# Kernel tuning notes

Hardware: AMD Instinct MI355X
Metric: run time of the kernel (lower is better)

Reference implementation:

```python
import jax, jax.numpy as jnp
import numpy as np
from jax import lax

NEG = -1e30  # finite stand-in for -inf (avoids NaN grads)
EPS = 1e-7   # keras backend epsilon used by ctc_batch_cost: log(y_pred + eps)

B, T, C, L = 64, 2048, 128, 256


def setup_inputs() -> dict:
    key = jax.random.key(0)
    k1, k2 = jax.random.split(key)
    # labels in [0, C-2]; blank index is C-1 per keras ctc_batch_cost convention
    y_true = jax.random.randint(k1, (B, L), 0, C - 1, dtype=jnp.int32).astype(jnp.int64)
    # y_pred are (unnormalized) per-frame class probabilities, as keras expects softmax output
    y_pred = jax.random.uniform(k2, (B, T, C), dtype=jnp.float32)
    return {"y_true": y_true, "y_pred": y_pred}


def _lse3(a, b, c):
    s = jnp.stack([a, b, c], axis=0)
    m = jnp.max(s, axis=0)
    return m + jnp.log(jnp.sum(jnp.exp(s - m), axis=0))


def _ctc_loss(y_true, y_pred):
    """Faithful jnp version of K.ctc_batch_cost with full input/label lengths."""
    b, t, c = y_pred.shape
    l = y_true.shape[1]
    blank = c - 1
    S = 2 * l + 1

    logp = jnp.log(y_pred + EPS)  # [B,T,C]

    labels = y_true.astype(jnp.int32)
    # extended label sequence: blank, l1, blank, l2, ..., blank  -> [B,S]
    ext = jnp.full((b, S), blank, dtype=jnp.int32).at[:, 1::2].set(labels)
    # gather per-frame log-probs of extended labels -> [B,T,S]
    lp_z = jnp.take_along_axis(logp, jnp.broadcast_to(ext[:, None, :], (b, t, S)), axis=2)

    # skip transition allowed at s if z[s] != blank and z[s] != z[s-2]
    ext_m2 = jnp.concatenate([jnp.full((b, 2), blank, jnp.int32), ext[:, :-2]], axis=1)
    skip = (ext != blank) & (ext != ext_m2) & (jnp.arange(S)[None, :] >= 2)  # [B,S]

    lp_tbs = jnp.transpose(lp_z, (1, 0, 2))  # [T,B,S]

    neg = jnp.full((b, S), NEG, dtype=logp.dtype)
    alpha0 = neg.at[:, 0].set(lp_tbs[0][:, 0]).at[:, 1].set(lp_tbs[0][:, 1])

    neg1 = jnp.full((b, 1), NEG, dtype=logp.dtype)
    neg2 = jnp.full((b, 2), NEG, dtype=logp.dtype)

    def step(alpha, lp_t):
        s1 = jnp.concatenate([neg1, alpha[:, :-1]], axis=1)
        s2 = jnp.where(skip, jnp.concatenate([neg2, alpha[:, :-2]], axis=1), NEG)
        new = _lse3(alpha, s1, s2) + lp_t
        return new, None

    alphaT, _ = lax.scan(step, alpha0, lp_tbs[1:])
    loss = -jnp.logaddexp(alphaT[:, -1], alphaT[:, -2])  # [B]
    return loss[:, None]  # keras ctc_batch_cost returns [B,1]


def reference(y_true, y_pred):
    return _ctc_loss(y_true, y_pred)
```

## Files before the change

### kernel.cpp

```cpp
#include <hip/hip_runtime.h>


#define B_ 64
#define T_ 2048
#define C_ 128
#define L_ 256
#define BLANK_ (C_ - 1)
#define EPSF 1e-7f
#define LN2F 0.69314718055994530942f
#define CH_ 16
#define SENT_ (-(1 << 28))

typedef __attribute__((address_space(1))) const void glob_cv;
typedef __attribute__((address_space(3))) void lds_v;
typedef __attribute__((address_space(3))) float lds_f;

__device__ __forceinline__ void gl2lds16(const void* g, void* l) {
    __builtin_amdgcn_global_load_lds((glob_cv*)g, (lds_v*)l, 16, 0, 0);
}

#define WAIT_VM(n) asm volatile("s_waitcnt vmcnt(" #n ")" ::: "memory")
#define DRAIN_LGKM() asm volatile("s_waitcnt lgkmcnt(0)" ::: "memory")

#define XS_(x) #x
#define XS(x) XS_(x)

#define FILLC(S, OFF) \
  "ds_read_b32 %[g" #S "b], %[cB] offset:" XS(OFF) "\n\t" \
  "ds_read_b32 %[g" #S "1], %[c1] offset:" XS(OFF) "\n\t" \
  "ds_read_b32 %[g" #S "3], %[c3] offset:" XS(OFF) "\n\t" \
  "ds_read_b32 %[g" #S "5], %[c5] offset:" XS(OFF) "\n\t" \
  "ds_read_b32 %[g" #S "7], %[c7] offset:" XS(OFF) "\n\t"
#define FILLN(S, OFF) \
  "ds_read_b32 %[g" #S "b], %[nB] offset:" XS(OFF) "\n\t" \
  "ds_read_b32 %[g" #S "1], %[n1] offset:" XS(OFF) "\n\t" \
  "ds_read_b32 %[g" #S "3], %[n3] offset:" XS(OFF) "\n\t" \
  "ds_read_b32 %[g" #S "5], %[n5] offset:" XS(OFF) "\n\t" \
  "ds_read_b32 %[g" #S "7], %[n7] offset:" XS(OFF) "\n\t"

#define STEPF(S, WN, FILLS) \
  "s_waitcnt lgkmcnt(" XS(WN) ")\n\t" \
  "v_mov_b32 %[t0], 0\n\t" \
  "v_add_f32 %[t1], 0x33d6bf95, %[g" #S "b]\n\t" \
  "v_add_f32 %[t2], 0x33d6bf95, %[g" #S "1]\n\t" \
  "v_add_f32 %[t3], 0x33d6bf95, %[g" #S "3]\n\t" \
  "v_add_f32 %[t4], 0x33d6bf95, %[g" #S "5]\n\t" \
  "v_add_f32 %[t5], 0x33d6bf95, %[g" #S "7]\n\t" \
  "v_mov_b32_dpp %[t0], %[va7] wave_shr:1 row_mask:0xf bank_mask:0xf\n\t" \
  "v_mul_f32 %[t0], %[t0], %[ups]\n\t" \
  "v_add_f32 %[t6], %[va0], %[va1]\n\t" \
  "v_fmac_f32 %[t6], %[m1], %[t0]\n\t" \
  "v_add_f32 %[va0], %[va0], %[t0]\n\t" \
  "v_mul_f32 %[va0], %[va0], %[t1]\n\t" \
  "v_add_f32 %[t7], %[va1], %[va2]\n\t" \
  "v_add_f32 %[t8], %[va2], %[va3]\n\t" \
  "v_fmac_f32 %[t8], %[m3], %[va1]\n\t" \
  "v_mul_f32 %[va1], %[t6], %[t2]\n\t" \
  "v_mul_f32 %[va2], %[t7], %[t1]\n\t" \
  "v_add_f32 %[t6], %[va3], %[va4]\n\t" \
  "v_add_f32 %[t7], %[va4], %[va5]\n\t" \
  "v_fmac_f32 %[t7], %[m5], %[va3]\n\t" \
  "v_mul_f32 %[va3], %[t8], %[t3]\n\t" \
  "v_mul_f32 %[va4], %[t6], %[t1]\n\t" \
  "v_add_f32 %[t6], %[va5], %[va6]\n\t" \
  "v_add_f32 %[t8], %[va6], %[va7]\n\t" \
  "v_fmac_f32 %[t8], %[m7], %[va5]\n\t" \
  "v_mul_f32 %[va5], %[t7], %[t4]\n\t" \
  "v_mul_f32 %[va6], %[t6], %[t1]\n\t" \
  "v_fmac_f32 %[va8], %[m8], %[va7]\n\t" \
  "v_mul_f32 %[va7], %[t8], %[t5]\n\t" \
  "v_mul_f32 %[va8], %[va8], %[t1]\n\t" \
  FILLS

#define STEPB(S, WN, FILLS) \
  "s_waitcnt lgkmcnt(" XS(WN) ")\n\t" \
  "v_mov_b32 %[t0], 0\n\t" \
  "v_add_f32 %[t1], 0x33d6bf95, %[g" #S "b]\n\t" \
  "v_add_f32 %[t2], 0x33d6bf95, %[g" #S "1]\n\t" \
  "v_add_f32 %[t3], 0x33d6bf95, %[g" #S "3]\n\t" \
  "v_add_f32 %[t4], 0x33d6bf95, %[g" #S "5]\n\t" \
  "v_add_f32 %[t5], 0x33d6bf95, %[g" #S "7]\n\t" \
  "v_mul_f32 %[va0], %[va0], %[t1]\n\t" \
  "v_mul_f32 %[va1], %[va1], %[t2]\n\t" \
  "v_mov_b32 %[t6], %[va0]\n\t" \
  "v_fmac_f32 %[t6], %[m1], %[va1]\n\t" \
  "v_mul_f32 %[va2], %[va2], %[t1]\n\t" \
  "v_mul_f32 %[va3], %[va3], %[t3]\n\t" \
  "v_mul_f32 %[va4], %[va4], %[t1]\n\t" \
  "v_mov_b32_dpp %[t0], %[t6] wave_shl:1 row_mask:0xf bank_mask:0xf\n\t" \
  "v_mul_f32 %[t0], %[t0], %[ups]\n\t" \
  "v_mul_f32 %[va5], %[va5], %[t4]\n\t" \
  "v_mul_f32 %[va6], %[va6], %[t1]\n\t" \
  "v_mul_f32 %[va7], %[va7], %[t5]\n\t" \
  "v_mul_f32 %[va8], %[va8], %[t1]\n\t" \
  "v_add_f32 %[t7], %[va1], %[va2]\n\t" \
  "v_fmac_f32 %[t7], %[m3], %[va3]\n\t" \
  "v_add_f32 %[va0], %[va0], %[va1]\n\t" \
  "v_add_f32 %[t8], %[va3], %[va4]\n\t" \
  "v_fmac_f32 %[t8], %[m5], %[va5]\n\t" \
  "v_add_f32 %[va2], %[va2], %[va3]\n\t" \
  "v_add_f32 %[t9], %[va5], %[va6]\n\t" \
  "v_fmac_f32 %[t9], %[m7], %[va7]\n\t" \
  "v_add_f32 %[va4], %[va4], %[va5]\n\t" \
  "v_add_f32 %[va6], %[va6], %[va7]\n\t" \
  "v_add_f32 %[va7], %[va7], %[t0]\n\t" \
  "v_fmac_f32 %[va7], %[m8], %[va8]\n\t" \
  "v_mov_b32 %[va1], %[t7]\n\t" \
  "v_mov_b32 %[va3], %[t8]\n\t" \
  "v_mov_b32 %[va5], %[t9]\n\t" \
  FILLS

#define BDY_HEAD \
  "v_max_f32 %[t1], %[va0], %[va1]\n\t" \
  "v_max_f32 %[t2], %[va2], %[va3]\n\t" \
  "v_max_f32 %[t3], %[va4], %[va5]\n\t" \
  "v_max_f32 %[t4], %[va6], %[va7]\n\t" \
  "v_max_f32 %[t1], %[t1], %[t2]\n\t" \
  "v_max_f32 %[t3], %[t3], %[t4]\n\t" \
  "v_max_f32 %[t1], %[t1], %[t3]\n\t" \
  "v_max_f32 %[t1], %[t1], %[va8]\n\t" \
  "v_cmp_ne_u32 vcc, 0, %[t1]\n\t" \
  "v_lshrrev_b32 %[t2], 23, %[t1]\n\t" \
  "v_sub_u32 %[t3], 0xfe, %[t2]\n\t" \
  "v_lshlrev_b32 %[t3], 23, %[t3]\n\t" \
  "v_cndmask_b32 %[t3], 1.0, %[t3], vcc\n\t" \
  "v_mul_f32 %[va0], %[va0], %[t3]\n\t" \
  "v_mul_f32 %[va1], %[va1], %[t3]\n\t" \
  "v_mul_f32 %[va2], %[va2], %[t3]\n\t" \
  "v_mul_f32 %[va3], %[va3], %[t3]\n\t" \
  "v_mul_f32 %[va4], %[va4], %[t3]\n\t" \
  "v_mul_f32 %[va5], %[va5], %[t3]\n\t" \
  "v_mul_f32 %[va6], %[va6], %[t3]\n\t" \
  "v_mul_f32 %[va7], %[va7], %[t3]\n\t" \
  "v_mul_f32 %[va8], %[va8], %[t3]\n\t" \
  "v_add_u32 %[t2], 0xffffff81, %[t2]\n\t" \
  "v_add_u32 %[t2], %[E], %[t2]\n\t" \
  "v_mov_b32 %[t4], 0xf0000000\n\t" \
  "v_cndmask_b32 %[E], %[t4], %[t2], vcc\n\t" \
  "v_mov_b32 %[t5], 0xf0000000\n\t" \
  "s_nop 1\n\t"
#define BDY_TAIL \
  "v_cmp_ne_u32 vcc, 0xf0000000, %[E]\n\t" \
  "v_cndmask_b32 %[E], %[t5], %[E], vcc\n\t" \
  "v_sub_u32 %[t6], %[t5], %[E]\n\t" \
  "v_max_i32 %[t6], 0xffffff82, %[t6]\n\t" \
  "v_min_i32 %[t6], 0x78, %[t6]\n\t" \
  "v_add_u32 %[t6], 0x7f, %[t6]\n\t" \
  "v_lshlrev_b32 %[ups], 23, %[t6]\n\t"
#define BDYF BDY_HEAD \
  "v_mov_b32_dpp %[t5], %[E] wave_shr:1 row_mask:0xf bank_mask:0xf\n\t" \
  BDY_TAIL
#define BDYB BDY_HEAD \
  "v_mov_b32_dpp %[t5], %[E] wave_shl:1 row_mask:0xf bank_mask:0xf\n\t" \
  BDY_TAIL

#define FWD_Q1 STEPF(0,15,FILLC(0,2048)) STEPF(1,15,FILLC(1,2560)) \
               STEPF(2,15,FILLC(2,3072)) STEPF(3,15,FILLC(3,3584)) BDYF
#define FWD_Q2 STEPF(0,15,FILLC(0,4096)) STEPF(1,15,FILLC(1,4608)) \
               STEPF(2,15,FILLC(2,5120)) STEPF(3,15,FILLC(3,5632)) BDYF
#define FWD_Q3 STEPF(0,15,FILLC(0,6144)) STEPF(1,15,FILLC(1,6656)) \
               STEPF(2,15,FILLC(2,7168)) STEPF(3,15,FILLC(3,7680)) BDYF
#define FWD_Q4 STEPF(0,15,FILLN(0,0))    STEPF(1,15,FILLN(1,512)) \
               STEPF(2,15,FILLN(2,1024)) STEPF(3,15,FILLN(3,1536)) BDYF
#define FWD_FULL_BODY FWD_Q1 FWD_Q2 FWD_Q3 FWD_Q4
#define FWD_FIRST_BODY \
  FILLC(1,512) FILLC(2,1024) FILLC(3,1536) FILLC(0,2048) \
  STEPF(1,15,FILLC(1,2560)) STEPF(2,15,FILLC(2,3072)) \
  STEPF(3,15,FILLC(3,3584)) BDYF \
  FWD_Q2 FWD_Q3 FWD_Q4
#define FWD_LAST_BODY FWD_Q1 FWD_Q2 FWD_Q3 \
  STEPF(0,15,"") STEPF(1,10,"") STEPF(2,5,"") STEPF(3,0,"") BDYF

#define BWD_Q1 STEPB(0,15,FILLC(0,5632)) STEPB(1,15,FILLC(1,5120)) \
               STEPB(2,15,FILLC(2,4608)) STEPB(3,15,FILLC(3,4096)) BDYB
#define BWD_Q2 STEPB(0,15,FILLC(0,3584)) STEPB(1,15,FILLC(1,3072)) \
               STEPB(2,15,FILLC(2,2560)) STEPB(3,15,FILLC(3,2048)) BDYB
#define BWD_Q3 STEPB(0,15,FILLC(0,1536)) STEPB(1,15,FILLC(1,1024)) \
               STEPB(2,15,FILLC(2,512))  STEPB(3,15,FILLC(3,0))    BDYB
#define BWD_Q4 STEPB(0,15,FILLN(0,7680)) STEPB(1,15,FILLN(1,7168)) \
               STEPB(2,15,FILLN(2,6656)) STEPB(3,15,FILLN(3,6144)) BDYB
#define BWD_FULL_BODY BWD_Q1 BWD_Q2 BWD_Q3 BWD_Q4
#define BWD_FIRST_BODY \
  FILLC(0,7680) FILLC(1,7168) FILLC(2,6656) FILLC(3,6144) \
  BWD_FULL_BODY
#define BWD_LAST_BODY BWD_Q1 BWD_Q2 BWD_Q3 \
  STEPB(0,15,"") STEPB(1,10,"") STEPB(2,5,"") STEPB(3,0,"") BDYB

#define ST_OUTS \
  [va0]"+&v"(a0),[va1]"+&v"(a1),[va2]"+&v"(a2),[va3]"+&v"(a3), \
  [va4]"+&v"(a4),[va5]"+&v"(a5),[va6]"+&v"(a6),[va7]"+&v"(a7), \
  [va8]"+&v"(a8),[E]"+&v"(E),[ups]"+&v"(ups), \
  [g0b]"+&v"(g0b),[g01]"+&v"(g01),[g03]"+&v"(g03),[g05]"+&v"(g05),[g07]"+&v"(g07), \
  [g1b]"+&v"(g1b),[g11]"+&v"(g11),[g13]"+&v"(g13),[g15]"+&v"(g15),[g17]"+&v"(g17), \
  [g2b]"+&v"(g2b),[g21]"+&v"(g21),[g23]"+&v"(g23),[g25]"+&v"(g25),[g27]"+&v"(g27), \
  [g3b]"+&v"(g3b),[g31]"+&v"(g31),[g33]"+&v"(g33),[g35]"+&v"(g35),[g37]"+&v"(g37), \
  [t0]"=&v"(t0),[t1]"=&v"(t1),[t2]"=&v"(t2),[t3]"=&v"(t3),[t4]"=&v"(t4), \
  [t5]"=&v"(t5),[t6]"=&v"(t6),[t7]"=&v"(t7),[t8]"=&v"(t8),[t9]"=&v"(t9)

#define RUN_CHUNK(BODY, XB,X1,X3,X5,X7, YB,Y1,Y3,Y5,Y7) \
  asm volatile(BODY : ST_OUTS \
    : [m1]"v"(m1f),[m3]"v"(m3f),[m5]"v"(m5f),[m7]"v"(m7f),[m8]"v"(m8f), \
      [cB]"v"(XB),[c1]"v"(X1),[c3]"v"(X3),[c5]"v"(X5),[c7]"v"(X7), \
      [nB]"v"(YB),[n1]"v"(Y1),[n3]"v"(Y3),[n5]"v"(Y5),[n7]"v"(Y7) \
    : "vcc","memory")

#define RUN_BDY(BODY) asm volatile(BODY : ST_OUTS :: "vcc","memory")

__launch_bounds__(128, 1)
__global__ void ctc_loss_kernel(const int* __restrict__ y_true,
                                const float* __restrict__ y_pred,
                                float* __restrict__ out) {
    const int b = blockIdx.x;
    const int tid = threadIdx.x;
    const int w = __builtin_amdgcn_readfirstlane(tid >> 6);
    const int l = tid & 63;

    __shared__ float ring[2][4][CH_ * C_];

    const int* __restrict__ lab = y_true + b * L_;
    const int4 lv = *(const int4*)(lab + 4 * l);
    const int e1 = lv.x, e3 = lv.y, e5 = lv.z, e7 = lv.w;
    const int em1 = (l > 0) ? lab[4 * l - 1] : -1;
    const float m1f = ((l > 0) && (e1 != em1)) ? 1.0f : 0.0f;
    const float m3f = (e3 != e1) ? 1.0f : 0.0f;
    const float m5f = (e5 != e3) ? 1.0f : 0.0f;
    const float m7f = (e7 != e5) ? 1.0f : 0.0f;
    const float m8f = (l == 63) ? 1.0f : 0.0f;

    const float* __restrict__ base = y_pred + (size_t)b * (T_ * C_);

    lds_f* lb = (lds_f*)&ring[0][0][0];
    lds_f* q0 = lb + w * 8192;
    lds_f* q1 = q0 + 2048;
    lds_f* q2 = q0 + 4096;
    lds_f* q3 = q0 + 6144;
    lds_f *cB0 = q0 + BLANK_, *c10 = q0 + e1, *c30 = q0 + e3,
          *c50 = q0 + e5, *c70 = q0 + e7;
    lds_f *cB1 = q1 + BLANK_, *c11 = q1 + e1, *c31 = q1 + e3,
          *c51 = q1 + e5, *c71 = q1 + e7;
    lds_f *cB2 = q2 + BLANK_, *c12 = q2 + e1, *c32 = q2 + e3,
          *c52 = q2 + e5, *c72 = q2 + e7;
    lds_f *cB3 = q3 + BLANK_, *c13 = q3 + e1, *c33 = q3 + e3,
          *c53 = q3 + e5, *c73 = q3 + e7;

    auto issueF = [&](int c, int buf) {
        const float* g = base + (size_t)c * CH_ * C_ + 4 * l;
#pragma unroll
        for (int i = 0; i < 8; ++i)
            gl2lds16(g + i * 256, &ring[0][buf][i * 256]);
    };
    auto issueB = [&](int qc, int buf) {
        const float* g = base + (size_t)(127 - qc) * CH_ * C_ + 4 * l;
#pragma unroll
        for (int i = 0; i < 8; ++i)
            gl2lds16(g + i * 256, &ring[1][buf][i * 256]);
    };

    float a0 = 0.f, a1 = 0.f, a2 = 0.f, a3 = 0.f, a4 = 0.f,
          a5 = 0.f, a6 = 0.f, a7 = 0.f, a8 = 0.f;
    int E = SENT_;
    float ups = 1.0f;
    float g0b = 0.f, g01 = 0.f, g03 = 0.f, g05 = 0.f, g07 = 0.f,
          g1b = 0.f, g11 = 0.f, g13 = 0.f, g15 = 0.f, g17 = 0.f,
          g2b = 0.f, g21 = 0.f, g23 = 0.f, g25 = 0.f, g27 = 0.f,
          g3b = 0.f, g31 = 0.f, g33 = 0.f, g35 = 0.f, g37 = 0.f;
    float t0, t1, t2, t3, t4, t5, t6, t7, t8, t9;

    if (w == 0) {
        issueF(0, 0); issueF(1, 1); issueF(2, 2);
        WAIT_VM(8);
        issueF(3, 3);
        {
            const float* rbf = &ring[0][0][0];
            const float i0 = rbf[BLANK_] + EPSF;
            const float i1 = rbf[e1] + EPSF;
            if (l == 0) { a0 = i0; a1 = i1; E = 0; }
        }
        RUN_BDY(BDYF);
        DRAIN_LGKM();
        RUN_CHUNK(FWD_FIRST_BODY, cB0,c10,c30,c50,c70, cB1,c11,c31,c51,c71);
        WAIT_VM(8); issueF(4, 0);
        RUN_CHUNK(FWD_FULL_BODY, cB1,c11,c31,c51,c71, cB2,c12,c32,c52,c72);
        WAIT_VM(8); issueF(5, 1);
        RUN_CHUNK(FWD_FULL_BODY, cB2,c12,c32,c52,c72, cB3,c13,c33,c53,c73);
        WAIT_VM(8); issueF(6, 2);
        RUN_CHUNK(FWD_FULL_BODY, cB3,c13,c33,c53,c73, cB0,c10,c30,c50,c70);
#pragma unroll 1
        for (int m = 1; m <= 14; ++m) {
            WAIT_VM(8); issueF(4 * m + 3, 3);
            RUN_CHUNK(FWD_FULL_BODY, cB0,c10,c30,c50,c70, cB1,c11,c31,c51,c71);
            WAIT_VM(8); issueF(4 * m + 4, 0);
            RUN_CHUNK(FWD_FULL_BODY, cB1,c11,c31,c51,c71, cB2,c12,c32,c52,c72);
            WAIT_VM(8); issueF(4 * m + 5, 1);
            RUN_CHUNK(FWD_FULL_BODY, cB2,c12,c32,c52,c72, cB3,c13,c33,c53,c73);
            WAIT_VM(8); issueF(4 * m + 6, 2);
            RUN_CHUNK(FWD_FULL_BODY, cB3,c13,c33,c53,c73, cB0,c10,c30,c50,c70);
        }
        WAIT_VM(8); issueF(63, 3);
        RUN_CHUNK(FWD_FULL_BODY, cB0,c10,c30,c50,c70, cB1,c11,c31,c51,c71);
        WAIT_VM(8);
        RUN_CHUNK(FWD_FULL_BODY, cB1,c11,c31,c51,c71, cB2,c12,c32,c52,c72);
        WAIT_VM(0);
        RUN_CHUNK(FWD_FULL_BODY, cB2,c12,c32,c52,c72, cB3,c13,c33,c53,c73);
        RUN_CHUNK(FWD_LAST_BODY, cB3,c13,c33,c53,c73, cB3,c13,c33,c53,c73);
    } else {
        issueB(0, 0); issueB(1, 1); issueB(2, 2);
        WAIT_VM(8);
        issueB(3, 3);
        if (l == 63) { a7 = 1.0f; a8 = 1.0f; E = 0; }
        RUN_BDY(BDYB);
        DRAIN_LGKM();
        RUN_CHUNK(BWD_FIRST_BODY, cB0,c10,c30,c50,c70, cB1,c11,c31,c51,c71);
        WAIT_VM(8); issueB(4, 0);
        RUN_CHUNK(BWD_FULL_BODY, cB1,c11,c31,c51,c71, cB2,c12,c32,c52,c72);
        WAIT_VM(8); issueB(5, 1);
        RUN_CHUNK(BWD_FULL_BODY, cB2,c12,c32,c52,c72, cB3,c13,c33,c53,c73);
        WAIT_VM(8); issueB(6, 2);
        RUN_CHUNK(BWD_FULL_BODY, cB3,c13,c33,c53,c73, cB0,c10,c30,c50,c70);
#pragma unroll 1
        for (int m = 1; m <= 14; ++m) {
            WAIT_VM(8); issueB(4 * m + 3, 3);
            RUN_CHUNK(BWD_FULL_BODY, cB0,c10,c30,c50,c70, cB1,c11,c31,c51,c71);
            WAIT_VM(8); issueB(4 * m + 4, 0);
            RUN_CHUNK(BWD_FULL_BODY, cB1,c11,c31,c51,c71, cB2,c12,c32,c52,c72);
            WAIT_VM(8); issueB(4 * m + 5, 1);
            RUN_CHUNK(BWD_FULL_BODY, cB2,c12,c32,c52,c72, cB3,c13,c33,c53,c73);
            WAIT_VM(8); issueB(4 * m + 6, 2);
            RUN_CHUNK(BWD_FULL_BODY, cB3,c13,c33,c53,c73, cB0,c10,c30,c50,c70);
        }
        WAIT_VM(8); issueB(63, 3);
        RUN_CHUNK(BWD_FULL_BODY, cB0,c10,c30,c50,c70, cB1,c11,c31,c51,c71);
        WAIT_VM(8);
        RUN_CHUNK(BWD_FULL_BODY, cB1,c11,c31,c51,c71, cB2,c12,c32,c52,c72);
        WAIT_VM(0);
        RUN_CHUNK(BWD_FULL_BODY, cB2,c12,c32,c52,c72, cB3,c13,c33,c53,c73);
        RUN_CHUNK(BWD_LAST_BODY, cB3,c13,c33,c53,c73, cB3,c13,c33,c53,c73);
        float* xf = &ring[1][0][0];
        xf[0 * 64 + l] = a0; xf[1 * 64 + l] = a1; xf[2 * 64 + l] = a2;
        xf[3 * 64 + l] = a3; xf[4 * 64 + l] = a4; xf[5 * 64 + l] = a5;
        xf[6 * 64 + l] = a6; xf[7 * 64 + l] = a7; xf[8 * 64 + l] = a8;
        ((int*)xf)[9 * 64 + l] = E;
    }

    __syncthreads();

    if (w == 0) {
        const float* xf = &ring[1][0][0];
        float sd = a0 * xf[0 * 64 + l];
        sd = fmaf(a1, xf[1 * 64 + l], sd);
        sd = fmaf(a2, xf[2 * 64 + l], sd);
        sd = fmaf(a3, xf[3 * 64 + l], sd);
        sd = fmaf(a4, xf[4 * 64 + l], sd);
        sd = fmaf(a5, xf[5 * 64 + l], sd);
        sd = fmaf(a6, xf[6 * 64 + l], sd);
        sd = fmaf(a7, xf[7 * 64 + l], sd);
        sd = fmaf(a8, xf[8 * 64 + l], sd);
        const int E2 = ((const int*)xf)[9 * 64 + l];
        const bool nz = (sd > 0.0f);
        int Es = nz ? (E + E2) : SENT_;
        int M = Es;
#pragma unroll
        for (int o = 32; o; o >>= 1) M = max(M, __shfl_xor(M, o));
        int d = Es - M;
        d = max(d, -126);
        float val = nz ? sd * __uint_as_float((unsigned)(d + 127) << 23) : 0.0f;
#pragma unroll
        for (int o = 32; o; o >>= 1) val += __shfl_xor(val, o);
        if (l == 0) out[b] = -(__logf(val) + (float)M * LN2F);
    }
}

extern "C" void kernel_launch(void* const* d_in, const int* in_sizes, int n_in,
                              void* d_out, int out_size, void* d_ws, size_t ws_size,
                              hipStream_t stream) {
    const int* y_true = (const int*)d_in[0];
    const float* y_pred = (const float*)d_in[1];
    float* out = (float*)d_out;
    ctc_loss_kernel<<<B_, 128, 0, stream>>>(y_true, y_pred, out);
}
```

Measured before the change: 184.6 us.

## Fold renormalization scale into next step's emission multiply and use fast boundary in late chunks

Adds a cheaper boundary renormalization variant that skips the zero/sentinel checks and uses max3. It defers applying the scale by folding it into the next step's emission factors through an FMA (g*sc + eps*sc). The fast boundary is used only in the later half of the time loop, where every lane is assumed to have left the all-zero sentinel state. It also removes extra moves and temporaries in the backward step and waits on LDS every other step. The risk is correctness if any lane still holds zeros or a sentinel exponent when the fast path begins.

```diff
diff --git a/kernel.cpp b/kernel.cpp
--- a/kernel.cpp
+++ b/kernel.cpp
@@ -24,6 +24,9 @@
 
 #define XS_(x) #x
 #define XS(x) XS_(x)
+
+#define WLG(n) "s_waitcnt lgkmcnt(" #n ")\n\t"
+#define NW ""
 
 #define FILLC(S, OFF) \
   "ds_read_b32 %[g" #S "b], %[cB] offset:" XS(OFF) "\n\t" \
@@ -38,16 +41,9 @@
   "ds_read_b32 %[g" #S "5], %[n5] offset:" XS(OFF) "\n\t" \
   "ds_read_b32 %[g" #S "7], %[n7] offset:" XS(OFF) "\n\t"
 
-#define STEPF(S, WN, FILLS) \
-  "s_waitcnt lgkmcnt(" XS(WN) ")\n\t" \
-  "v_mov_b32 %[t0], 0\n\t" \
-  "v_add_f32 %[t1], 0x33d6bf95, %[g" #S "b]\n\t" \
-  "v_add_f32 %[t2], 0x33d6bf95, %[g" #S "1]\n\t" \
-  "v_add_f32 %[t3], 0x33d6bf95, %[g" #S "3]\n\t" \
-  "v_add_f32 %[t4], 0x33d6bf95, %[g" #S "5]\n\t" \
-  "v_add_f32 %[t5], 0x33d6bf95, %[g" #S "7]\n\t" \
-  "v_mov_b32_dpp %[t0], %[va7] wave_shr:1 row_mask:0xf bank_mask:0xf\n\t" \
-  "v_mul_f32 %[t0], %[t0], %[ups]\n\t" \
+#define FCORE \
+  "v_mov_b32_dpp %[z0], %[va7] wave_shr:1 row_mask:0xf bank_mask:0xf\n\t" \
+  "v_mul_f32 %[t0], %[z0], %[ups]\n\t" \
   "v_add_f32 %[t6], %[va0], %[va1]\n\t" \
   "v_fmac_f32 %[t6], %[m1], %[t0]\n\t" \
   "v_add_f32 %[va0], %[va0], %[t0]\n\t" \
@@ -69,45 +65,68 @@
   "v_mul_f32 %[va6], %[t6], %[t1]\n\t" \
   "v_fmac_f32 %[va8], %[m8], %[va7]\n\t" \
   "v_mul_f32 %[va7], %[t8], %[t5]\n\t" \
-  "v_mul_f32 %[va8], %[va8], %[t1]\n\t" \
-  FILLS
-
-#define STEPB(S, WN, FILLS) \
-  "s_waitcnt lgkmcnt(" XS(WN) ")\n\t" \
-  "v_mov_b32 %[t0], 0\n\t" \
+  "v_mul_f32 %[va8], %[va8], %[t1]\n\t"
+
+#define STEPF(S, W, FILLS) W \
   "v_add_f32 %[t1], 0x33d6bf95, %[g" #S "b]\n\t" \
   "v_add_f32 %[t2], 0x33d6bf95, %[g" #S "1]\n\t" \
   "v_add_f32 %[t3], 0x33d6bf95, %[g" #S "3]\n\t" \
   "v_add_f32 %[t4], 0x33d6bf95, %[g" #S "5]\n\t" \
   "v_add_f32 %[t5], 0x33d6bf95, %[g" #S "7]\n\t" \
+  FCORE FILLS
+
+#define STEPF1(S, W, FILLS) W \
+  "v_fma_f32 %[t1], %[g" #S "b], %[sc], %[esc]\n\t" \
+  "v_fma_f32 %[t2], %[g" #S "1], %[sc], %[esc]\n\t" \
+  "v_fma_f32 %[t3], %[g" #S "3], %[sc], %[esc]\n\t" \
+  "v_fma_f32 %[t4], %[g" #S "5], %[sc], %[esc]\n\t" \
+  "v_fma_f32 %[t5], %[g" #S "7], %[sc], %[esc]\n\t" \
+  FCORE \
+  "v_mov_b32 %[ups], %[upn]\n\t" \
+  FILLS
+
+#define BCORE(UPSREG) \
   "v_mul_f32 %[va0], %[va0], %[t1]\n\t" \
   "v_mul_f32 %[va1], %[va1], %[t2]\n\t" \
-  "v_mov_b32 %[t6], %[va0]\n\t" \
-  "v_fmac_f32 %[t6], %[m1], %[va1]\n\t" \
+  "v_fma_f32 %[t6], %[m1], %[va1], %[va0]\n\t" \
   "v_mul_f32 %[va2], %[va2], %[t1]\n\t" \
   "v_mul_f32 %[va3], %[va3], %[t3]\n\t" \
   "v_mul_f32 %[va4], %[va4], %[t1]\n\t" \
-  "v_mov_b32_dpp %[t0], %[t6] wave_shl:1 row_mask:0xf bank_mask:0xf\n\t" \
-  "v_mul_f32 %[t0], %[t0], %[ups]\n\t" \
   "v_mul_f32 %[va5], %[va5], %[t4]\n\t" \
   "v_mul_f32 %[va6], %[va6], %[t1]\n\t" \
   "v_mul_f32 %[va7], %[va7], %[t5]\n\t" \
   "v_mul_f32 %[va8], %[va8], %[t1]\n\t" \
-  "v_add_f32 %[t7], %[va1], %[va2]\n\t" \
-  "v_fmac_f32 %[t7], %[m3], %[va3]\n\t" \
+  "v_mov_b32_dpp %[z0], %[t6] wave_shl:1 row_mask:0xf bank_mask:0xf\n\t" \
+  "v_mul_f32 %[t0], %[z0], " UPSREG "\n\t" \
   "v_add_f32 %[va0], %[va0], %[va1]\n\t" \
-  "v_add_f32 %[t8], %[va3], %[va4]\n\t" \
-  "v_fmac_f32 %[t8], %[m5], %[va5]\n\t" \
+  "v_add_f32 %[va1], %[va1], %[va2]\n\t" \
+  "v_fmac_f32 %[va1], %[m3], %[va3]\n\t" \
   "v_add_f32 %[va2], %[va2], %[va3]\n\t" \
-  "v_add_f32 %[t9], %[va5], %[va6]\n\t" \
-  "v_fmac_f32 %[t9], %[m7], %[va7]\n\t" \
+  "v_add_f32 %[va3], %[va3], %[va4]\n\t" \
+  "v_fmac_f32 %[va3], %[m5], %[va5]\n\t" \
   "v_add_f32 %[va4], %[va4], %[va5]\n\t" \
+  "v_add_f32 %[va5], %[va5], %[va6]\n\t" \
+  "v_fmac_f32 %[va5], %[m7], %[va7]\n\t" \
   "v_add_f32 %[va6], %[va6], %[va7]\n\t" \
   "v_add_f32 %[va7], %[va7], %[t0]\n\t" \
-  "v_fmac_f32 %[va7], %[m8], %[va8]\n\t" \
-  "v_mov_b32 %[va1], %[t7]\n\t" \
-  "v_mov_b32 %[va3], %[t8]\n\t" \
-  "v_mov_b32 %[va5], %[t9]\n\t" \
+  "v_fmac_f32 %[va7], %[m8], %[va8]\n\t"
+
+#define STEPB(S, W, FILLS) W \
+  "v_add_f32 %[t1], 0x33d6bf95, %[g" #S "b]\n\t" \
+  "v_add_f32 %[t2], 0x33d6bf95, %[g" #S "1]\n\t" \
+  "v_add_f32 %[t3], 0x33d6bf95, %[g" #S "3]\n\t" \
+  "v_add_f32 %[t4], 0x33d6bf95, %[g" #S "5]\n\t" \
+  "v_add_f32 %[t5], 0x33d6bf95, %[g" #S "7]\n\t" \
+  BCORE("%[ups]") FILLS
+
+#define STEPB1(S, W, FILLS) W \
+  "v_fma_f32 %[t1], %[g" #S "b], %[sc], %[esc]\n\t" \
+  "v_fma_f32 %[t2], %[g" #S "1], %[sc], %[esc]\n\t" \
+  "v_fma_f32 %[t3], %[g" #S "3], %[sc], %[esc]\n\t" \
+  "v_fma_f32 %[t4], %[g" #S "5], %[sc], %[esc]\n\t" \
+  "v_fma_f32 %[t5], %[g" #S "7], %[sc], %[esc]\n\t" \
+  BCORE("%[upn]") \
+  "v_mov_b32 %[ups], %[upn]\n\t" \
   FILLS
 
 #define BDY_HEAD \
@@ -146,56 +165,90 @@
   "v_max_i32 %[t6], 0xffffff82, %[t6]\n\t" \
   "v_min_i32 %[t6], 0x78, %[t6]\n\t" \
   "v_add_u32 %[t6], 0x7f, %[t6]\n\t" \
-  "v_lshlrev_b32 %[ups], 23, %[t6]\n\t"
-#define BDYF BDY_HEAD \
+  "v_lshlrev_b32 %[ups], 23, %[t6]\n\t" \
+  "v_mov_b32 %[sc], 1.0\n\t" \
+  "v_mov_b32 %[esc], 0x33d6bf95\n\t" \
+  "v_mov_b32 %[upn], %[ups]\n\t"
+#define BDYF_FULL BDY_HEAD \
   "v_mov_b32_dpp %[t5], %[E] wave_shr:1 row_mask:0xf bank_mask:0xf\n\t" \
   BDY_TAIL
-#define BDYB BDY_HEAD \
+#define BDYB_FULL BDY_HEAD \
   "v_mov_b32_dpp %[t5], %[E] wave_shl:1 row_mask:0xf bank_mask:0xf\n\t" \
   BDY_TAIL
 
-#define FWD_Q1 STEPF(0,15,FILLC(0,2048)) STEPF(1,15,FILLC(1,2560)) \
-               STEPF(2,15,FILLC(2,3072)) STEPF(3,15,FILLC(3,3584)) BDYF
-#define FWD_Q2 STEPF(0,15,FILLC(0,4096)) STEPF(1,15,FILLC(1,4608)) \
-               STEPF(2,15,FILLC(2,5120)) STEPF(3,15,FILLC(3,5632)) BDYF
-#define FWD_Q3 STEPF(0,15,FILLC(0,6144)) STEPF(1,15,FILLC(1,6656)) \
-               STEPF(2,15,FILLC(2,7168)) STEPF(3,15,FILLC(3,7680)) BDYF
-#define FWD_Q4 STEPF(0,15,FILLN(0,0))    STEPF(1,15,FILLN(1,512)) \
-               STEPF(2,15,FILLN(2,1024)) STEPF(3,15,FILLN(3,1536)) BDYF
-#define FWD_FULL_BODY FWD_Q1 FWD_Q2 FWD_Q3 FWD_Q4
+#define FBDY_HEAD \
+  "v_max3_f32 %[t1], %[va0], %[va1], %[va2]\n\t" \
+  "v_max3_f32 %[t2], %[va3], %[va4], %[va5]\n\t" \
+  "v_max3_f32 %[t3], %[va6], %[va7], %[va8]\n\t" \
+  "v_max3_f32 %[t1], %[t1], %[t2], %[t3]\n\t" \
+  "v_lshrrev_b32 %[t2], 23, %[t1]\n\t" \
+  "v_add_u32 %[t4], 0xffffff81, %[t2]\n\t" \
+  "v_add_u32 %[E], %[E], %[t4]\n\t" \
+  "v_sub_u32 %[t3], 0xfe, %[t2]\n\t" \
+  "v_lshlrev_b32 %[sc], 23, %[t3]\n\t" \
+  "v_mul_f32 %[esc], 0x33d6bf95, %[sc]\n\t"
+#define FBDY_TAIL \
+  "v_sub_u32 %[t4], %[t5], %[E]\n\t" \
+  "v_max_i32 %[t4], 0xffffff82, %[t4]\n\t" \
+  "v_min_i32 %[t4], 0x78, %[t4]\n\t" \
+  "v_add_u32 %[t4], 0x7f, %[t4]\n\t" \
+  "v_lshlrev_b32 %[upn], 23, %[t4]\n\t"
+#define BDYF_FAST FBDY_HEAD \
+  "v_mov_b32_dpp %[t5], %[E] wave_shr:1 row_mask:0xf bank_mask:0xf\n\t" \
+  FBDY_TAIL
+#define BDYB_FAST FBDY_HEAD \
+  "v_mov_b32_dpp %[t5], %[E] wave_shl:1 row_mask:0xf bank_mask:0xf\n\t" \
+  FBDY_TAIL
+
+#define FQ1(BDY) STEPF1(0,WLG(10),FILLC(0,2048)) STEPF(1,NW,FILLC(1,2560)) \
+                 STEPF(2,WLG(10),FILLC(2,3072)) STEPF(3,NW,FILLC(3,3584)) BDY
+#define FQ2(BDY) STEPF1(0,WLG(10),FILLC(0,4096)) STEPF(1,NW,FILLC(1,4608)) \
+                 STEPF(2,WLG(10),FILLC(2,5120)) STEPF(3,NW,FILLC(3,5632)) BDY
+#define FQ3(BDY) STEPF1(0,WLG(10),FILLC(0,6144)) STEPF(1,NW,FILLC(1,6656)) \
+                 STEPF(2,WLG(10),FILLC(2,7168)) STEPF(3,NW,FILLC(3,7680)) BDY
+#define FQ4(BDY) STEPF1(0,WLG(10),FILLN(0,0))    STEPF(1,NW,FILLN(1,512)) \
+                 STEPF(2,WLG(10),FILLN(2,1024)) STEPF(3,NW,FILLN(3,1536)) BDY
+
+#define FWD_FULL_BODY FQ1(BDYF_FULL) FQ2(BDYF_FULL) FQ3(BDYF_FULL) FQ4(BDYF_FULL)
+#define FWD_FAST_BODY FQ1(BDYF_FAST) FQ2(BDYF_FAST) FQ3(BDYF_FAST) FQ4(BDYF_FAST)
 #define FWD_FIRST_BODY \
   FILLC(1,512) FILLC(2,1024) FILLC(3,1536) FILLC(0,2048) \
-  STEPF(1,15,FILLC(1,2560)) STEPF(2,15,FILLC(2,3072)) \
-  STEPF(3,15,FILLC(3,3584)) BDYF \
-  FWD_Q2 FWD_Q3 FWD_Q4
-#define FWD_LAST_BODY FWD_Q1 FWD_Q2 FWD_Q3 \
-  STEPF(0,15,"") STEPF(1,10,"") STEPF(2,5,"") STEPF(3,0,"") BDYF
-
-#define BWD_Q1 STEPB(0,15,FILLC(0,5632)) STEPB(1,15,FILLC(1,5120)) \
-               STEPB(2,15,FILLC(2,4608)) STEPB(3,15,FILLC(3,4096)) BDYB
-#define BWD_Q2 STEPB(0,15,FILLC(0,3584)) STEPB(1,15,FILLC(1,3072)) \
-               STEPB(2,15,FILLC(2,2560)) STEPB(3,15,FILLC(3,2048)) BDYB
-#define BWD_Q3 STEPB(0,15,FILLC(0,1536)) STEPB(1,15,FILLC(1,1024)) \
-               STEPB(2,15,FILLC(2,512))  STEPB(3,15,FILLC(3,0))    BDYB
-#define BWD_Q4 STEPB(0,15,FILLN(0,7680)) STEPB(1,15,FILLN(1,7168)) \
-               STEPB(2,15,FILLN(2,6656)) STEPB(3,15,FILLN(3,6144)) BDYB
-#define BWD_FULL_BODY BWD_Q1 BWD_Q2 BWD_Q3 BWD_Q4
+  STEPF1(1,WLG(10),FILLC(1,2560)) STEPF(2,NW,FILLC(2,3072)) \
+  STEPF(3,WLG(10),FILLC(3,3584)) BDYF_FULL \
+  FQ2(BDYF_FULL) FQ3(BDYF_FULL) FQ4(BDYF_FULL)
+#define FWD_LAST_BODY FQ1(BDYF_FAST) FQ2(BDYF_FAST) FQ3(BDYF_FAST) \
+  STEPF1(0,WLG(10),"") STEPF(1,NW,"") STEPF(2,WLG(5),"") STEPF(3,WLG(0),"") \
+  BDYF_FULL
+
+#define BQ1(BDY) STEPB1(0,WLG(10),FILLC(0,5632)) STEPB(1,NW,FILLC(1,5120)) \
+                 STEPB(2,WLG(10),FILLC(2,4608)) STEPB(3,NW,FILLC(3,4096)) BDY
+#define BQ2(BDY) STEPB1(0,WLG(10),FILLC(0,3584)) STEPB(1,NW,FILLC(1,3072)) \
+                 STEPB(2,WLG(10),FILLC(2,2560)) STEPB(3,NW,FILLC(3,2048)) BDY
+#define BQ3(BDY) STEPB1(0,WLG(10),FILLC(0,1536)) STEPB(1,NW,FILLC(1,1024)) \
+                 STEPB(2,WLG(10),FILLC(2,512))  STEPB(3,NW,FILLC(3,0))    BDY
+#define BQ4(BDY) STEPB1(0,WLG(10),FILLN(0,7680)) STEPB(1,NW,FILLN(1,7168)) \
+                 STEPB(2,WLG(10),FILLN(2,6656)) STEPB(3,NW,FILLN(3,6144)) BDY
+
+#define BWD_FULL_BODY BQ1(BDYB_FULL) BQ2(BDYB_FULL) BQ3(BDYB_FULL) BQ4(BDYB_FULL)
+#define BWD_FAST_BODY BQ1(BDYB_FAST) BQ2(BDYB_FAST) BQ3(BDYB_FAST) BQ4(BDYB_FAST)
 #define BWD_FIRST_BODY \
   FILLC(0,7680) FILLC(1,7168) FILLC(2,6656) FILLC(3,6144) \
   BWD_FULL_BODY
-#define BWD_LAST_BODY BWD_Q1 BWD_Q2 BWD_Q3 \
-  STEPB(0,15,"") STEPB(1,10,"") STEPB(2,5,"") STEPB(3,0,"") BDYB
+#define BWD_LAST_BODY BQ1(BDYB_FAST) BQ2(BDYB_FAST) BQ3(BDYB_FAST) \
+  STEPB1(0,WLG(10),"") STEPB(1,NW,"") STEPB(2,WLG(5),"") STEPB(3,WLG(0),"") \
+  BDYB_FULL
 
 #define ST_OUTS \
   [va0]"+&v"(a0),[va1]"+&v"(a1),[va2]"+&v"(a2),[va3]"+&v"(a3), \
   [va4]"+&v"(a4),[va5]"+&v"(a5),[va6]"+&v"(a6),[va7]"+&v"(a7), \
-  [va8]"+&v"(a8),[E]"+&v"(E),[ups]"+&v"(ups), \
+  [va8]"+&v"(a8),[E]"+&v"(E),[ups]"+&v"(ups),[upn]"+&v"(upn), \
+  [sc]"+&v"(sc),[esc]"+&v"(esc),[z0]"+&v"(z0), \
   [g0b]"+&v"(g0b),[g01]"+&v"(g01),[g03]"+&v"(g03),[g05]"+&v"(g05),[g07]"+&v"(g07), \
   [g1b]"+&v"(g1b),[g11]"+&v"(g11),[g13]"+&v"(g13),[g15]"+&v"(g15),[g17]"+&v"(g17), \
   [g2b]"+&v"(g2b),[g21]"+&v"(g21),[g23]"+&v"(g23),[g25]"+&v"(g25),[g27]"+&v"(g27), \
   [g3b]"+&v"(g3b),[g31]"+&v"(g31),[g33]"+&v"(g33),[g35]"+&v"(g35),[g37]"+&v"(g37), \
   [t0]"=&v"(t0),[t1]"=&v"(t1),[t2]"=&v"(t2),[t3]"=&v"(t3),[t4]"=&v"(t4), \
-  [t5]"=&v"(t5),[t6]"=&v"(t6),[t7]"=&v"(t7),[t8]"=&v"(t8),[t9]"=&v"(t9)
+  [t5]"=&v"(t5),[t6]"=&v"(t6),[t7]"=&v"(t7),[t8]"=&v"(t8)
 
 #define RUN_CHUNK(BODY, XB,X1,X3,X5,X7, YB,Y1,Y3,Y5,Y7) \
   asm volatile(BODY : ST_OUTS \
@@ -259,12 +312,12 @@
     float a0 = 0.f, a1 = 0.f, a2 = 0.f, a3 = 0.f, a4 = 0.f,
           a5 = 0.f, a6 = 0.f, a7 = 0.f, a8 = 0.f;
     int E = SENT_;
-    float ups = 1.0f;
+    float ups = 1.0f, upn = 1.0f, sc = 1.0f, esc = EPSF, z0 = 0.0f;
     float g0b = 0.f, g01 = 0.f, g03 = 0.f, g05 = 0.f, g07 = 0.f,
           g1b = 0.f, g11 = 0.f, g13 = 0.f, g15 = 0.f, g17 = 0.f,
           g2b = 0.f, g21 = 0.f, g23 = 0.f, g25 = 0.f, g27 = 0.f,
           g3b = 0.f, g31 = 0.f, g33 = 0.f, g35 = 0.f, g37 = 0.f;
-    float t0, t1, t2, t3, t4, t5, t6, t7, t8, t9;
+    float t0, t1, t2, t3, t4, t5, t6, t7, t8;
 
     if (w == 0) {
         issueF(0, 0); issueF(1, 1); issueF(2, 2);
@@ -276,7 +329,7 @@
             const float i1 = rbf[e1] + EPSF;
             if (l == 0) { a0 = i0; a1 = i1; E = 0; }
         }
-        RUN_BDY(BDYF);
+        RUN_BDY(BDYF_FULL);
         DRAIN_LGKM();
         RUN_CHUNK(FWD_FIRST_BODY, cB0,c10,c30,c50,c70, cB1,c11,c31,c51,c71);
         WAIT_VM(8); issueF(4, 0);
@@ -286,7 +339,7 @@
         WAIT_VM(8); issueF(6, 2);
         RUN_CHUNK(FWD_FULL_BODY, cB3,c13,c33,c53,c73, cB0,c10,c30,c50,c70);
 #pragma unroll 1
-        for (int m = 1; m <= 14; ++m) {
+        for (int m = 1; m <= 6; ++m) {
             WAIT_VM(8); issueF(4 * m + 3, 3);
             RUN_CHUNK(FWD_FULL_BODY, cB0,c10,c30,c50,c70, cB1,c11,c31,c51,c71);
             WAIT_VM(8); issueF(4 * m + 4, 0);
@@ -296,19 +349,30 @@
             WAIT_VM(8); issueF(4 * m + 6, 2);
             RUN_CHUNK(FWD_FULL_BODY, cB3,c13,c33,c53,c73, cB0,c10,c30,c50,c70);
         }
+#pragma unroll 1
+        for (int m = 7; m <= 14; ++m) {
+            WAIT_VM(8); issueF(4 * m + 3, 3);
+            RUN_CHUNK(FWD_FAST_BODY, cB0,c10,c30,c50,c70, cB1,c11,c31,c51,c71);
+            WAIT_VM(8); issueF(4 * m + 4, 0);
+            RUN_CHUNK(FWD_FAST_BODY, cB1,c11,c31,c51,c71, cB2,c12,c32,c52,c72);
+            WAIT_VM(8); issueF(4 * m + 5, 1);
+            RUN_CHUNK(FWD_FAST_BODY, cB2,c12,c32,c52,c72, cB3,c13,c33,c53,c73);
+            WAIT_VM(8); issueF(4 * m + 6, 2);
+            RUN_CHUNK(FWD_FAST_BODY, cB3,c13,c33,c53,c73, cB0,c10,c30,c50,c70);
+        }
         WAIT_VM(8); issueF(63, 3);
-        RUN_CHUNK(FWD_FULL_BODY, cB0,c10,c30,c50,c70, cB1,c11,c31,c51,c71);
+        RUN_CHUNK(FWD_FAST_BODY, cB0,c10,c30,c50,c70, cB1,c11,c31,c51,c71);
         WAIT_VM(8);
-        RUN_CHUNK(FWD_FULL_BODY, cB1,c11,c31,c51,c71, cB2,c12,c32,c52,c72);
+        RUN_CHUNK(FWD_FAST_BODY, cB1,c11,c31,c51,c71, cB2,c12,c32,c52,c72);
         WAIT_VM(0);
-        RUN_CHUNK(FWD_FULL_BODY, cB2,c12,c32,c52,c72, cB3,c13,c33,c53,c73);
+        RUN_CHUNK(FWD_FAST_BODY, cB2,c12,c32,c52,c72, cB3,c13,c33,c53,c73);
         RUN_CHUNK(FWD_LAST_BODY, cB3,c13,c33,c53,c73, cB3,c13,c33,c53,c73);
     } else {
         issueB(0, 0); issueB(1, 1); issueB(2, 2);
         WAIT_VM(8);
         issueB(3, 3);
         if (l == 63) { a7 = 1.0f; a8 = 1.0f; E = 0; }
-        RUN_BDY(BDYB);
+        RUN_BDY(BDYB_FULL);
         DRAIN_LGKM();
         RUN_CHUNK(BWD_FIRST_BODY, cB0,c10,c30,c50,c70, cB1,c11,c31,c51,c71);
         WAIT_VM(8); issueB(4, 0);
@@ -318,7 +382,7 @@
         WAIT_VM(8); issueB(6, 2);
         RUN_CHUNK(BWD_FULL_BODY, cB3,c13,c33,c53,c73, cB0,c10,c30,c50,c70);
 #pragma unroll 1
-        for (int m = 1; m <= 14; ++m) {
+        for (int m = 1; m <= 6; ++m) {
             WAIT_VM(8); issueB(4 * m + 3, 3);
             RUN_CHUNK(BWD_FULL_BODY, cB0,c10,c30,c50,c70, cB1,c11,c31,c51,c71);
             WAIT_VM(8); issueB(4 * m + 4, 0);
@@ -328,12 +392,23 @@
             WAIT_VM(8); issueB(4 * m + 6, 2);
             RUN_CHUNK(BWD_FULL_BODY, cB3,c13,c33,c53,c73, cB0,c10,c30,c50,c70);
         }
+#pragma unroll 1
+        for (int m = 7; m <= 14; ++m) {
+            WAIT_VM(8); issueB(4 * m + 3, 3);
+            RUN_CHUNK(BWD_FAST_BODY, cB0,c10,c30,c50,c70, cB1,c11,c31,c51,c71);
+            WAIT_VM(8); issueB(4 * m + 4, 0);
+            RUN_CHUNK(BWD_FAST_BODY, cB1,c11,c31,c51,c71, cB2,c12,c32,c52,c72);
+            WAIT_VM(8); issueB(4 * m + 5, 1);
+            RUN_CHUNK(BWD_FAST_BODY, cB2,c12,c32,c52,c72, cB3,c13,c33,c53,c73);
+            WAIT_VM(8); issueB(4 * m + 6, 2);
+            RUN_CHUNK(BWD_FAST_BODY, cB3,c13,c33,c53,c73, cB0,c10,c30,c50,c70);
+        }
         WAIT_VM(8); issueB(63, 3);
-        RUN_CHUNK(BWD_FULL_BODY, cB0,c10,c30,c50,c70, cB1,c11,c31,c51,c71);
+        RUN_CHUNK(BWD_FAST_BODY, cB0,c10,c30,c50,c70, cB1,c11,c31,c51,c71);
         WAIT_VM(8);
-        RUN_CHUNK(BWD_FULL_BODY, cB1,c11,c31,c51,c71, cB2,c12,c32,c52,c72);
+        RUN_CHUNK(BWD_FAST_BODY, cB1,c11,c31,c51,c71, cB2,c12,c32,c52,c72);
         WAIT_VM(0);
-        RUN_CHUNK(BWD_FULL_BODY, cB2,c12,c32,c52,c72, cB3,c13,c33,c53,c73);
+        RUN_CHUNK(BWD_FAST_BODY, cB2,c12,c32,c52,c72, cB3,c13,c33,c53,c73);
         RUN_CHUNK(BWD_LAST_BODY, cB3,c13,c33,c53,c73, cB3,c13,c33,c53,c73);
         float* xf = &ring[1][0][0];
         xf[0 * 64 + l] = a0; xf[1 * 64 + l] = a1; xf[2 * 64 + l] = a2;
```

Measured after the change: 171.8 us. -7.0%, faster.
